# Kernel tuning notes

Hardware: AMD Instinct MI355X
Metric: run time of the kernel (lower is better)

## Reference

```python
import jax, jax.numpy as jnp
import numpy as np
from jax import lax

B, T_IN, T_TASK = 1024, 512, 64
D_IN, D_TASK_FEAT, H, D_OUT = 9, 9, 100, 9


def setup_inputs() -> dict:
    key = jax.random.key(0)
    ks = jax.random.split(key, 8)
    s = 0.1
    return {
        "input": jax.random.normal(ks[0], (B, T_IN, D_IN), jnp.float32),
        "task": jax.random.normal(ks[1], (B, T_TASK, D_TASK_FEAT), jnp.float32),
        "W_in": jax.random.normal(ks[2], (D_IN, 9), jnp.float32) * s,
        "b_in": jnp.zeros((9,), jnp.float32),
        "W_task": jax.random.normal(ks[3], (D_TASK_FEAT, 9), jnp.float32) * s,
        "b_task": jnp.zeros((9,), jnp.float32),
        "W_x": jax.random.normal(ks[4], (9, 4 * H), jnp.float32) * s,
        "W_h": jax.random.normal(ks[5], (H, 4 * H), jnp.float32) * s,
        "b_lstm": jnp.zeros((4 * H,), jnp.float32),
        "W_out": jax.random.normal(ks[6], (H, D_OUT), jnp.float32) * s,
        "b_out": jnp.zeros((D_OUT,), jnp.float32),
    }


def reference(input, task, W_in, b_in, W_task, b_task, W_x, W_h, b_lstm, W_out, b_out):
    # Dense encoders with relu
    x = jax.nn.relu(jnp.einsum("btf,fd->btd", input, W_in) + b_in)      # [B,T1,9]
    t = jax.nn.relu(jnp.einsum("btf,fd->btd", task, W_task) + b_task)   # [B,T2,9]
    seq = jnp.concatenate([x, t], axis=1)                                # [B,T1+T2,9] (axis=1 = time)

    b = seq.shape[0]
    h0 = jnp.zeros((b, H), seq.dtype)
    c0 = jnp.zeros((b, H), seq.dtype)

    # Precompute input contributions for all timesteps (one big GEMM)
    zx = jnp.einsum("btf,fg->btg", seq, W_x) + b_lstm                    # [B,T,4H]

    def step(carry, zxt):
        h, c = carry
        z = zxt + h @ W_h                                                # [B,4H]
        i, f, g, o = jnp.split(z, 4, axis=-1)                            # Keras gate order i,f,c,o
        i = jax.nn.sigmoid(i)
        f = jax.nn.sigmoid(f)
        g = jnp.tanh(g)
        o = jax.nn.sigmoid(o)
        c = f * c + i * g
        h = o * jnp.tanh(c)
        return (h, c), h

    _, hs = lax.scan(step, (h0, c0), zx.transpose(1, 0, 2))              # hs: [T,B,H]
    hs = hs.transpose(1, 0, 2)                                           # [B,T,H]

    logits = jnp.einsum("bth,hd->btd", hs, W_out) + b_out
    return jax.nn.softmax(logits, axis=-1)
```

## Files before the change

### kernel.cpp

```cpp
#include <hip/hip_runtime.h>


#define NTHR 1024

typedef _Float16 half8 __attribute__((ext_vector_type(8)));
typedef float    f32x4 __attribute__((ext_vector_type(4)));

struct __align__(16) SM {
  _Float16 Y[2][4][144];
};

__device__ __forceinline__ float fast_sigmoid(float x) {
  return __builtin_amdgcn_rcpf(1.f + __expf(-x));
}
__device__ __forceinline__ float fast_tanh(float x) {
  return fmaf(2.f, __builtin_amdgcn_rcpf(1.f + __expf(-2.f * x)), -1.f);
}

__device__ __forceinline__ float wld(int k, int n,
                                     const float* __restrict__ Wh,
                                     const float* __restrict__ Wx,
                                     const float* __restrict__ bl) {
  if (k < 100)  return Wh[k * 400 + n];
  if (k < 109)  return Wx[(k - 100) * 400 + n];
  if (k == 109) return bl[n];
  return 0.f;
}

__device__ __forceinline__ float wproj(int k, int m,
                                       const float* __restrict__ Wo,
                                       const float* __restrict__ bo) {
  if (m >= 9)   return 0.f;
  if (k < 100)  return Wo[k * 9 + m];
  if (k == 109) return bo[m];
  return 0.f;
}

__device__ __forceinline__ void sync_lds() {
  asm volatile("s_waitcnt lgkmcnt(0)" ::: "memory");
  __builtin_amdgcn_s_barrier();
  asm volatile("" ::: "memory");
}

__global__ __launch_bounds__(NTHR, 4)
void lstm_fused(const float* __restrict__ g_input,
                const float* __restrict__ g_task,
                const float* __restrict__ g_Win,
                const float* __restrict__ g_bin,
                const float* __restrict__ g_Wtask,
                const float* __restrict__ g_btask,
                const float* __restrict__ g_Wx,
                const float* __restrict__ g_Wh,
                const float* __restrict__ g_bl,
                const float* __restrict__ g_Wout,
                const float* __restrict__ g_bout,
                float* __restrict__ g_out)
{
  __shared__ SM L;
  const int tid  = threadIdx.x;
  const int bg0  = blockIdx.x * 4;
  const int wv   = tid >> 6;
  const int lane = tid & 63;
  const int q    = lane >> 4;
  const int nl   = lane & 15;
  const int hi   = lane >> 4;
  const int xr_  = nl >> 2;
  const int ab   = nl & 3;

  for (int i = tid; i < 2 * 4 * 144; i += NTHR)
    ((_Float16*)L.Y)[i] = ((i % 144) == 109) ? (_Float16)1.f : (_Float16)0.f;

  const int NR    = (wv < 12) ? 2 : (wv == 12) ? 1 : 0;
  const int NTF   = (wv == 15) ? 1 : NR;
  const int tbase = (wv < 12) ? wv * 2 : 24;

  half8 Af[2][4];
  {
    const int gate = ab;
    const int Uin  = xr_;
#pragma unroll
    for (int ti = 0; ti < 2; ++ti) {
      if (ti < NTF) {
        const bool proj = (wv == 15);
        const int n = gate * 100 + (tbase + ti) * 4 + Uin;
#pragma unroll
        for (int kc = 0; kc < 4; ++kc) {
#pragma unroll
          for (int j = 0; j < 8; ++j) {
            const int k = kc * 32 + q * 8 + j;
            Af[ti][kc][j] = (_Float16)(proj ? wproj(k, nl, g_Wout, g_bout)
                                            : wld(k, n, g_Wh, g_Wx, g_bl));
          }
        }
      }
    }
  }

  const int aU = (tbase + ((NR == 2) ? (xr_ & 1) : 0)) * 4 + hi;
  float c_state = 0.f;

  const int sl  = lane - 28;
  const int stb = (sl >= 0) ? sl / 9 : 0;
  const int stf = (sl >= 0) ? sl % 9 : 0;
  float we_in[9], we_task[9], be_in = 0.f, be_task = 0.f;
  if (wv == 14) {
#pragma unroll
    for (int ff = 0; ff < 9; ++ff) {
      we_in[ff]   = g_Win[ff * 9 + stf];
      we_task[ff] = g_Wtask[ff * 9 + stf];
    }
    be_in = g_bin[stf]; be_task = g_btask[stf];
  }
  float xrA[9], xrB[9];

  auto LOADX = [&](float* xr, int tt) {
    const float* src = (tt < 512)
      ? g_input + ((long)(bg0 + stb) * 512 + tt) * 9
      : g_task  + ((long)(bg0 + stb) * 64 + (tt - 512)) * 9;
#pragma unroll
    for (int ff = 0; ff < 9; ++ff) xr[ff] = src[ff];
  };
  auto ENC9 = [&](const float* xr, const float (&w)[9], float b) -> float {
    float a0 = b, a1 = 0.f, a2 = 0.f;
    a0 = fmaf(xr[0], w[0], a0); a1 = fmaf(xr[1], w[1], a1); a2 = fmaf(xr[2], w[2], a2);
    a0 = fmaf(xr[3], w[3], a0); a1 = fmaf(xr[4], w[4], a1); a2 = fmaf(xr[5], w[5], a2);
    a0 = fmaf(xr[6], w[6], a0); a1 = fmaf(xr[7], w[7], a1); a2 = fmaf(xr[8], w[8], a2);
    return (a0 + a1) + a2;
  };
  auto ENCSTEP = [&](const float* xr, int tt) {
    float a;
    if (tt < 512) a = ENC9(xr, we_in, be_in);
    else          a = ENC9(xr, we_task, be_task);
    L.Y[tt & 1][stb][100 + stf] = (_Float16)fmaxf(a, 0.f);
  };
  auto ACT = [&](int p, const float* zv) {
    const float gi = fast_sigmoid(zv[0]);
    const float gf = fast_sigmoid(zv[1]);
    const float gg = fast_tanh(zv[2]);
    const float go = fast_sigmoid(zv[3]);
    c_state = fmaf(gf, c_state, gi * gg);
    L.Y[p ^ 1][ab][aU] = (_Float16)(go * fast_tanh(c_state));
  };
  auto SMAX = [&](f32x4 v, int tout) {
    float e0 = __expf(v[0]), e1 = __expf(v[1]), e2 = __expf(v[2]), e3 = __expf(v[3]);
    if (hi == 2) { e1 = 0.f; e2 = 0.f; e3 = 0.f; }
    if (hi == 3) { e0 = 0.f; e1 = 0.f; e2 = 0.f; e3 = 0.f; }
    const float pl = (e0 + e1) + (e2 + e3);
    const float s1 = pl + __uint_as_float(__builtin_amdgcn_ds_swizzle(__float_as_uint(pl), 0x401F));
    const float ss = s1 + __shfl_xor(s1, 32, 64);
    const float rs = __builtin_amdgcn_rcpf(ss);
    if (hi < 3) {
      float* dst = g_out + ((long)(bg0 + ab) * 576 + tout) * 9 + 4 * hi;
      dst[0] = e0 * rs;
      if (hi < 2) { dst[1] = e1 * rs; dst[2] = e2 * rs; dst[3] = e3 * rs; }
    }
  };

  sync_lds();

  if (wv == 14 && sl >= 0) {
    float x0[9];
    LOADX(x0, 0);
    L.Y[0][stb][100 + stf] = (_Float16)fmaxf(ENC9(x0, we_in, be_in), 0.f);
    LOADX(xrB, 1);
    LOADX(xrA, 2);
  }
  sync_lds();

  for (int t = 0; t < 576; ++t) {
    const int p = t & 1;
    half8 Bv[4];
    f32x4 acc[2];
    if (NTF > 0) {
#pragma unroll
      for (int kc = 0; kc < 4; ++kc)
        Bv[kc] = *(const half8*)&L.Y[p][ab][kc * 32 + q * 8];
#pragma unroll
      for (int ti = 0; ti < 2; ++ti) {
        if (ti < NTF) {
          acc[ti] = (f32x4)0.f;
#pragma unroll
          for (int kc = 0; kc < 4; ++kc)
            acc[ti] = __builtin_amdgcn_mfma_f32_16x16x32_f16(Af[ti][kc], Bv[kc], acc[ti], 0, 0, 0);
        }
      }
    }
    if (NR > 0) {
      if (xr_ < NR) {
        float zv[4];
#pragma unroll
        for (int g = 0; g < 4; ++g)
          zv[g] = (NR == 2 && (xr_ & 1)) ? acc[1][g] : acc[0][g];
        ACT(p, zv);
      }
    } else if (wv == 15) {
      if (xr_ == 0 && t > 0) SMAX(acc[0], t - 1);
    } else if (wv == 14) {
      if (sl >= 0 && t + 1 < 576) {
        if (t & 1) { ENCSTEP(xrA, t + 1); if (t + 3 < 576) LOADX(xrA, t + 3); }
        else       { ENCSTEP(xrB, t + 1); if (t + 3 < 576) LOADX(xrB, t + 3); }
      }
    }
    sync_lds();
  }

  if (wv == 15) {
    half8 Bv[4];
#pragma unroll
    for (int kc = 0; kc < 4; ++kc)
      Bv[kc] = *(const half8*)&L.Y[0][ab][kc * 32 + q * 8];
    f32x4 a0 = (f32x4)0.f;
#pragma unroll
    for (int kc = 0; kc < 4; ++kc)
      a0 = __builtin_amdgcn_mfma_f32_16x16x32_f16(Af[0][kc], Bv[kc], a0, 0, 0, 0);
    if (xr_ == 0) SMAX(a0, 575);
  }
}

extern "C" void kernel_launch(void* const* d_in, const int* in_sizes, int n_in,
                              void* d_out, int out_size, void* d_ws, size_t ws_size,
                              hipStream_t stream) {
  const float* input  = (const float*)d_in[0];
  const float* task   = (const float*)d_in[1];
  const float* W_in   = (const float*)d_in[2];
  const float* b_in   = (const float*)d_in[3];
  const float* W_task = (const float*)d_in[4];
  const float* b_task = (const float*)d_in[5];
  const float* W_x    = (const float*)d_in[6];
  const float* W_h    = (const float*)d_in[7];
  const float* b_lstm = (const float*)d_in[8];
  const float* W_out  = (const float*)d_in[9];
  const float* b_out  = (const float*)d_in[10];
  float* out = (float*)d_out;

  lstm_fused<<<256, NTHR, 0, stream>>>(input, task, W_in, b_in, W_task, b_task,
                                       W_x, W_h, b_lstm, W_out, b_out, out);
}
```

Measured before the change: 437.3 us.

## Split recurrent MFMA into two phases overlapping activation with partial GEMM

Restructures the per-timestep loop into three barrier-separated phases. Waves 0-7 apply their activations first. The second half of the hidden units (waves 8-12) compute activations concurrently with the first-half K-chunk MFMAs, and the remaining K chunks are issued after a barrier. The goal is to shorten the serial critical path of each recurrent step by overlapping gate math with matrix work. In exchange there are three barriers per step instead of one, plus a more intricate timing of which hidden units are ready for which K chunk.

Result: slower. 668.0 us (+52.8%).

```diff
diff --git a/kernel.cpp b/kernel.cpp
--- a/kernel.cpp
+++ b/kernel.cpp
@@ -133,13 +133,13 @@
     else          a = ENC9(xr, we_task, be_task);
     L.Y[tt & 1][stb][100 + stf] = (_Float16)fmaxf(a, 0.f);
   };
-  auto ACT = [&](int p, const float* zv) {
+  auto ACT = [&](int dstp, const float* zv) {
     const float gi = fast_sigmoid(zv[0]);
     const float gf = fast_sigmoid(zv[1]);
     const float gg = fast_tanh(zv[2]);
     const float go = fast_sigmoid(zv[3]);
     c_state = fmaf(gf, c_state, gi * gg);
-    L.Y[p ^ 1][ab][aU] = (_Float16)(go * fast_tanh(c_state));
+    L.Y[dstp][ab][aU] = (_Float16)(go * fast_tanh(c_state));
   };
   auto SMAX = [&](f32x4 v, int tout) {
     float e0 = __expf(v[0]), e1 = __expf(v[1]), e2 = __expf(v[2]), e3 = __expf(v[3]);
@@ -162,39 +162,74 @@
     float x0[9];
     LOADX(x0, 0);
     L.Y[0][stb][100 + stf] = (_Float16)fmaxf(ENC9(x0, we_in, be_in), 0.f);
-    LOADX(xrB, 1);
+    LOADX(x0, 1);
+    L.Y[1][stb][100 + stf] = (_Float16)fmaxf(ENC9(x0, we_in, be_in), 0.f);
     LOADX(xrA, 2);
-  }
-  sync_lds();
-
-  for (int t = 0; t < 576; ++t) {
+    LOADX(xrB, 3);
+  }
+  sync_lds();
+
+  f32x4 acc[2];
+  if (NTF > 0) {
+    half8 Bv[4];
+#pragma unroll
+    for (int kc = 0; kc < 4; ++kc)
+      Bv[kc] = *(const half8*)&L.Y[0][ab][kc * 32 + q * 8];
+#pragma unroll
+    for (int ti = 0; ti < 2; ++ti) {
+      if (ti < NTF) {
+        acc[ti] = (f32x4)0.f;
+#pragma unroll
+        for (int kc = 0; kc < 4; ++kc)
+          acc[ti] = __builtin_amdgcn_mfma_f32_16x16x32_f16(Af[ti][kc], Bv[kc], acc[ti], 0, 0, 0);
+      }
+    }
+  }
+  sync_lds();
+
+  for (int t = 1; t < 576; ++t) {
     const int p = t & 1;
-    half8 Bv[4];
-    f32x4 acc[2];
+    if (wv < 8) {
+      float zv[4];
+#pragma unroll
+      for (int g = 0; g < 4; ++g)
+        zv[g] = (xr_ & 1) ? acc[1][g] : acc[0][g];
+      if (xr_ < 2) ACT(p, zv);
+    } else if (wv == 15) {
+      if (xr_ == 0 && t > 1) SMAX(acc[0], t - 2);
+    }
+    sync_lds();
     if (NTF > 0) {
-#pragma unroll
-      for (int kc = 0; kc < 4; ++kc)
-        Bv[kc] = *(const half8*)&L.Y[p][ab][kc * 32 + q * 8];
+      float zvh[4];
+      const bool acth = (wv >= 8 && wv <= 12);
+      if (acth) {
+#pragma unroll
+        for (int g = 0; g < 4; ++g)
+          zvh[g] = (NR == 2 && (xr_ & 1)) ? acc[1][g] : acc[0][g];
+      }
+      const half8 B0 = *(const half8*)&L.Y[p][ab][q * 8];
+      const half8 B1 = *(const half8*)&L.Y[p][ab][32 + q * 8];
 #pragma unroll
       for (int ti = 0; ti < 2; ++ti) {
         if (ti < NTF) {
           acc[ti] = (f32x4)0.f;
-#pragma unroll
-          for (int kc = 0; kc < 4; ++kc)
-            acc[ti] = __builtin_amdgcn_mfma_f32_16x16x32_f16(Af[ti][kc], Bv[kc], acc[ti], 0, 0, 0);
+          acc[ti] = __builtin_amdgcn_mfma_f32_16x16x32_f16(Af[ti][0], B0, acc[ti], 0, 0, 0);
+          acc[ti] = __builtin_amdgcn_mfma_f32_16x16x32_f16(Af[ti][1], B1, acc[ti], 0, 0, 0);
         }
       }
-    }
-    if (NR > 0) {
-      if (xr_ < NR) {
-        float zv[4];
-#pragma unroll
-        for (int g = 0; g < 4; ++g)
-          zv[g] = (NR == 2 && (xr_ & 1)) ? acc[1][g] : acc[0][g];
-        ACT(p, zv);
-      }
-    } else if (wv == 15) {
-      if (xr_ == 0 && t > 0) SMAX(acc[0], t - 1);
+      if (acth && xr_ < NR) ACT(p, zvh);
+    }
+    sync_lds();
+    if (NTF > 0) {
+      const half8 B2 = *(const half8*)&L.Y[p][ab][64 + q * 8];
+      const half8 B3 = *(const half8*)&L.Y[p][ab][96 + q * 8];
+#pragma unroll
+      for (int ti = 0; ti < 2; ++ti) {
+        if (ti < NTF) {
+          acc[ti] = __builtin_amdgcn_mfma_f32_16x16x32_f16(Af[ti][2], B2, acc[ti], 0, 0, 0);
+          acc[ti] = __builtin_amdgcn_mfma_f32_16x16x32_f16(Af[ti][3], B3, acc[ti], 0, 0, 0);
+        }
+      }
     } else if (wv == 14) {
       if (sl >= 0 && t + 1 < 576) {
         if (t & 1) { ENCSTEP(xrA, t + 1); if (t + 3 < 576) LOADX(xrA, t + 3); }
@@ -204,6 +239,22 @@
     sync_lds();
   }
 
+  if (wv < 8) {
+    float zv[4];
+#pragma unroll
+    for (int g = 0; g < 4; ++g)
+      zv[g] = (xr_ & 1) ? acc[1][g] : acc[0][g];
+    if (xr_ < 2) ACT(0, zv);
+  } else if (wv >= 8 && wv <= 12) {
+    float zv[4];
+#pragma unroll
+    for (int g = 0; g < 4; ++g)
+      zv[g] = (NR == 2 && (xr_ & 1)) ? acc[1][g] : acc[0][g];
+    if (xr_ < NR) ACT(0, zv);
+  } else if (wv == 15) {
+    if (xr_ == 0) SMAX(acc[0], 574);
+  }
+  sync_lds();
   if (wv == 15) {
     half8 Bv[4];
 #pragma unroll
```
